# Performance work log

Hardware: AMD Instinct MI355X
Metric: run time of the kernel (lower is better)

Reference implementation:

```python
import jax, jax.numpy as jnp
import numpy as np

BETA = 0.25  # commitment_beta


def setup_inputs() -> dict:
    key = jax.random.key(0)
    k1, k2 = jax.random.split(key)
    x = jax.random.normal(k1, (16, 256, 32, 32), dtype=jnp.float32)
    # codebook weight: (n_embed + 1, embed_dim); last row is the padding idx (zeros)
    weight = jax.random.normal(k2, (8193, 256), dtype=jnp.float32) * 0.05
    weight = weight.at[-1].set(0.0)
    return {"x": x, "weight": weight}


def reference(x, weight):
    # Eval-mode forward of VectorQuantize2 (accept_image_fmap=True, no EMA update).
    B, C, H, W = x.shape
    xf = jnp.transpose(x, (0, 2, 3, 1)).reshape(B, H * W, C)  # b (h w) c
    emb = weight[:-1]  # [N, C], drop padding row
    # squared euclidean distance; argmin identical to torch.cdist argmin
    d2 = (
        jnp.sum(xf * xf, axis=-1, keepdims=True)
        - 2.0 * jnp.einsum("bnc,kc->bnk", xf, emb)
        + jnp.sum(emb * emb, axis=-1)
    )  # [B, HW, N]
    code = jnp.argmin(d2, axis=-1)  # [B, HW]
    x_q = emb[code]  # [B, HW, C]
    loss = BETA * jnp.mean((jax.lax.stop_gradient(x_q) - xf) ** 2) + jnp.mean(
        (x_q - jax.lax.stop_gradient(xf)) ** 2
    )
    # straight-through estimator
    xq_st = xf + jax.lax.stop_gradient(x_q - xf)
    xq_out = jnp.transpose(xq_st.reshape(B, H, W, C), (0, 3, 1, 2))  # b c h w
    code_out = code.reshape(B, H, W)
    return xq_out, loss, code_out
```

## Files before the change

### kernel.cpp

```cpp
#include <hip/hip_runtime.h>
#include <hip/hip_bf16.h>


#define N_ROWS   16384
#define KCODES   8192
#define DIM      256
#define LOSS_OFF 4194304
#define CODE_OFF 4194305
#define MARGIN_ACC 0.006f

typedef _Float16 half8  __attribute__((ext_vector_type(8)));
typedef _Float16 half4v __attribute__((ext_vector_type(4)));
typedef float    float4v __attribute__((ext_vector_type(4)));
typedef unsigned long long u64;

__device__ __forceinline__ unsigned umax32(unsigned a, unsigned b) { return a > b ? a : b; }
__device__ __forceinline__ unsigned umin32(unsigned a, unsigned b) { return a < b ? a : b; }
__device__ __forceinline__ void gll16(const _Float16* g, _Float16* l) {
  __builtin_amdgcn_global_load_lds((const __attribute__((address_space(1))) void*)g,
                                   (__attribute__((address_space(3))) void*)l, 16, 0, 0);
}


__global__ __launch_bounds__(256) void k_prep(const float* __restrict__ x, _Float16* __restrict__ xh,
                                              const float* __restrict__ wt, _Float16* __restrict__ eh,
                                              float* __restrict__ en2c) {
  __shared__ __align__(16) _Float16 ls[8192];
  __shared__ float es[32];
  int t = threadIdx.x;
  if (blockIdx.x < 256) {
    int blk = blockIdx.x;
    int row = t & 63;
    int s   = t >> 6;
    int r   = blk * 64 + row;
    int b   = r >> 10;
    int n   = r & 1023;
    const float* xb = x + (size_t)b * 262144 + n;
    int r7 = r & 7, rl = r & 127;
    size_t tb = (size_t)(r >> 7) * 32768;
    for (int j = 0; j < 8; ++j) {
      int g = s + 4 * j;
      int chunk = g >> 3, kg = g & 7;
      half8 h;
#pragma unroll
      for (int i = 0; i < 8; ++i) h[i] = (_Float16)xb[(size_t)(g * 8 + i) * 1024];
      int p = kg ^ r7;
      *(half8*)&xh[tb + (size_t)chunk * 8192 + rl * 64 + p * 8] = h;
    }
  } else {
    int blk  = blockIdx.x - 256;
    int lane = t & 63, wv = t >> 6;
    int k0 = blk * 32;
    const float* wb = wt + (size_t)k0 * 256;
    for (int i = 0; i < 8; ++i) {
      int lin = i * 1024 + t * 4;
      float4v v = *(const float4v*)&wb[lin];
      half4v h; float ss = 0.f;
#pragma unroll
      for (int j = 0; j < 4; ++j) { h[j] = (_Float16)v[j]; ss = fmaf(v[j], v[j], ss); }
      *(half4v*)&ls[lin] = h;
#pragma unroll
      for (int d = 32; d; d >>= 1) ss += __shfl_xor(ss, d);
      if (lane == 0) es[i * 4 + wv] = ss;
    }
    __syncthreads();
    size_t tb = (size_t)(k0 >> 7) * 32768;
    for (int i = 0; i < 4; ++i) {
      int u = i * 256 + t;
      int code_l = u >> 5;
      int cu = u & 31, chunk = cu >> 3, p = cu & 7;
      int kgl = k0 + code_l;
      int kg = p ^ (kgl & 7);
      half8 h = *(half8*)&ls[code_l * 256 + chunk * 64 + kg * 8];
      *(half8*)&eh[tb + (size_t)chunk * 8192 + (size_t)(kgl & 127) * 64 + p * 8] = h;
    }
    if (t < 32) en2c[k0 + t] = 32.0f - 0.5f * es[t];
  }
}

__global__ __launch_bounds__(256) void k_gemm(const _Float16* __restrict__ xh, const _Float16* __restrict__ eh,
                                              const float* __restrict__ en2c,
                                              u64* __restrict__ top2) {
  __shared__ __align__(16) _Float16 As[8192];
  __shared__ __align__(16) _Float16 Bs[8192];
  int t    = threadIdx.x;
  int bx   = blockIdx.x;
  int by   = blockIdx.y;
  int lane = t & 63, w = t >> 6;
  int wr = w & 1, wc = w >> 1;
  int ln15 = lane & 15, q = lane >> 4;
  int q4 = q * 4;

  const _Float16* Ag = eh + (size_t)bx * 32768;
  const _Float16* Bg = xh + (size_t)by * 32768;

  int kwave = bx * 128 + wr * 64;
  float4v cin[4];
#pragma unroll
  for (int mi = 0; mi < 4; ++mi) cin[mi] = *(const float4v*)&en2c[kwave + mi * 16 + q4];

  float4v acc[4][4];
#pragma unroll
  for (int mi = 0; mi < 4; ++mi)
#pragma unroll
    for (int ni = 0; ni < 4; ++ni) acc[mi][ni] = cin[mi];

  int so = (w * 64 + lane) * 8;
  int lo = w * 512;

  for (int ch = 0; ch < 4; ++ch) {
    if (ch) __syncthreads();
    const _Float16* ac = Ag + ch * 8192;
    const _Float16* bc = Bg + ch * 8192;
#pragma unroll
    for (int i = 0; i < 4; ++i) {
      gll16(ac + i * 2048 + so, As + i * 2048 + lo);
      gll16(bc + i * 2048 + so, Bs + i * 2048 + lo);
    }
    __syncthreads();
#pragma unroll
    for (int ks = 0; ks < 2; ++ks) {
      half8 af[4], bf[4];
#pragma unroll
      for (int mi = 0; mi < 4; ++mi) {
        int row = wr * 64 + mi * 16 + ln15;
        af[mi] = *(const half8*)&As[(row * 8 + ((ks * 4 + q) ^ (row & 7))) * 8];
      }
#pragma unroll
      for (int ni = 0; ni < 4; ++ni) {
        int row = wc * 64 + ni * 16 + ln15;
        bf[ni] = *(const half8*)&Bs[(row * 8 + ((ks * 4 + q) ^ (row & 7))) * 8];
      }
#pragma unroll
      for (int mi = 0; mi < 4; ++mi)
#pragma unroll
        for (int ni = 0; ni < 4; ++ni)
          acc[mi][ni] = __builtin_amdgcn_mfma_f32_16x16x32_f16(af[mi], bf[ni], acc[mi][ni], 0, 0, 0);
    }
  }

  __syncthreads();
  u64* ep = (u64*)(void*)As;
  int ibase = wr * 64 + q4;

#pragma unroll
  for (int ni = 0; ni < 4; ++ni) {
    unsigned hi[8], lo2[8];
#pragma unroll
    for (int j = 0; j < 8; ++j) {
      int mi = j >> 1, rb = (j & 1) * 2;
      unsigned p0 = (__float_as_uint(acc[mi][ni][rb])     & 0xFFFFFF80u) | (unsigned)(ibase + mi * 16 + rb);
      unsigned p1 = (__float_as_uint(acc[mi][ni][rb + 1]) & 0xFFFFFF80u) | (unsigned)(ibase + mi * 16 + rb + 1);
      hi[j] = umax32(p0, p1); lo2[j] = umin32(p0, p1);
    }
#pragma unroll
    for (int st = 4; st; st >>= 1)
#pragma unroll
      for (int j = 0; j < 8; ++j) if (j < st) {
        unsigned nb = umax32(hi[j], hi[j + st]);
        unsigned ns = umax32(umin32(hi[j], hi[j + st]), umax32(lo2[j], lo2[j + st]));
        hi[j] = nb; lo2[j] = ns;
      }
    unsigned b = hi[0], s = lo2[0];
#pragma unroll
    for (int d = 16; d < 64; d <<= 1) {
      unsigned ob = __shfl_xor(b, d);
      unsigned os = __shfl_xor(s, d);
      unsigned ns = umax32(umin32(b, ob), umax32(s, os));
      b = umax32(b, ob); s = ns;
    }
    if (q == 0) {
      int rl = wc * 64 + ni * 16 + ln15;
      ep[rl * 2 + wr] = ((u64)b << 32) | s;
    }
  }
  __syncthreads();
  if (t < 128) {
    u64 A = ep[t * 2 + 0], B = ep[t * 2 + 1];
    unsigned a0 = (unsigned)(A >> 32), a1 = (unsigned)A;
    unsigned b0 = (unsigned)(B >> 32), b1 = (unsigned)B;
    unsigned best = umax32(a0, b0);
    unsigned sec  = umax32(umin32(a0, b0), umax32(a1, b1));
    top2[((size_t)by * 128 + t) * 64 + bx] = ((u64)best << 32) | sec;
  }
}

__global__ __launch_bounds__(256) void k_refine_out(const u64* __restrict__ top2,
                                                    const float* __restrict__ x, const float* __restrict__ w,
                                                    float* __restrict__ out,
                                                    float* __restrict__ lacc, unsigned* __restrict__ cnt) {
  __shared__ float ec[32 * 261];
  __shared__ int   cds[32];
  __shared__ float part[4];
  int t    = threadIdx.x;
  int lane = t & 63, wv = t >> 6;
  int blk  = blockIdx.x;
  int row0 = blk * 32;
  int b = row0 >> 10, n0 = row0 & 1023;

  for (int j = 0; j < 8; ++j) {
    int rl  = wv + 4 * j;
    int row = row0 + rl;
    u64 e = top2[(size_t)row * 64 + lane];
    unsigned hi = (unsigned)(e >> 32), lo = (unsigned)e;
    unsigned mx = hi;
#pragma unroll
    for (int d = 1; d < 64; d <<= 1) mx = umax32(mx, __shfl_xor(mx, d));
    float fm = __uint_as_float(mx & 0xFFFFFF80u);
    float th = fm - MARGIN_ACC;
    bool c0 = __uint_as_float(hi & 0xFFFFFF80u) >= th;
    bool c1 = __uint_as_float(lo & 0xFFFFFF80u) >= th;
    u64 bal0 = __ballot(c0), bal1 = __ballot(c1);
    int kbest;
    if (__popcll(bal0) + __popcll(bal1) <= 1) {
      int l0 = __ffsll((unsigned long long)__ballot(hi == mx)) - 1;
      kbest = l0 * 128 + (int)(__shfl(hi, l0) & 127u);
    } else {
      int n = row & 1023;
      const float* xr = x + (size_t)b * 262144 + n;
      float4v ex;
#pragma unroll
      for (int i = 0; i < 4; ++i) ex[i] = xr[(size_t)(lane * 4 + i) * 1024];
      double bs = 1e300; int bk = 0x7fffffff;
      for (int pass = 0; pass < 2; ++pass) {
        u64 bal = pass ? bal1 : bal0;
        unsigned src = pass ? lo : hi;
        while (bal) {
          int l = __ffsll((unsigned long long)bal) - 1;
          bal &= bal - 1;
          int kc = l * 128 + (int)(__shfl(src, l) & 127u);
          float4v wv4 = *(const float4v*)&w[(size_t)kc * DIM + lane * 4];
          double s = 0.0;
#pragma unroll
          for (int i = 0; i < 4; ++i) { double ev = (double)wv4[i]; s += ev * (ev - 2.0 * (double)ex[i]); }
#pragma unroll
          for (int d = 1; d < 64; d <<= 1) s += __shfl_xor(s, d);
          if (s < bs || (s == bs && kc < bk)) { bs = s; bk = kc; }
        }
      }
      kbest = bk;
    }
    if (lane == 0) { cds[rl] = kbest; out[CODE_OFF + row] = (float)kbest; }
  }
  __syncthreads();

  {
    int rr = t >> 6;
    int c4 = (t & 63) * 4;
    for (int j = 0; j < 8; ++j) {
      int r = rr + 4 * j;
      float4v v = *(const float4v*)&w[(size_t)cds[r] * DIM + c4];
#pragma unroll
      for (int i = 0; i < 4; ++i) ec[r * 261 + c4 + i] = v[i];
    }
  }
  __syncthreads();
  float ls = 0.f;
  int r2 = t & 31;
  int cg = t >> 5;
  const size_t base = (size_t)b * 262144 + n0 + r2;
  for (int j = 0; j < 32; ++j) {
    int c = cg * 32 + j;
    float v  = ec[r2 * 261 + c];
    size_t a = base + (size_t)c * 1024;
    float xv = x[a];
    out[a] = v;
    float d = v - xv;
    ls = fmaf(d, d, ls);
  }
#pragma unroll
  for (int d = 32; d; d >>= 1) ls += __shfl_xor(ls, d);
  if (lane == 0) part[wv] = ls;
  __syncthreads();
  if (t == 0) {
    atomicAdd(lacc, part[0] + part[1] + part[2] + part[3]);
    __threadfence();
    unsigned old = atomicAdd(cnt, 1u);
    if (old == 511u) {
      __threadfence();
      out[LOSS_OFF] = 1.25f * (*(volatile float*)lacc) / 4194304.0f;
    }
  }
}

extern "C" void kernel_launch(void* const* d_in, const int* in_sizes, int n_in,
                              void* d_out, int out_size, void* d_ws, size_t ws_size,
                              hipStream_t stream) {
  const float* x = (const float*)d_in[0];
  const float* w = (const float*)d_in[1];
  float* out = (float*)d_out;
  char* ws = (char*)d_ws;
  _Float16* xh   = (_Float16*)(ws);
  _Float16* eh   = (_Float16*)(ws + 8388608);
  float*    en2c = (float*)(ws + 12582912);
  u64*      top2 = (u64*)(ws + 12615680);
  float*    lacc = (float*)(ws + 21004288);
  unsigned* cnt  = (unsigned*)(ws + 21004292);

  hipMemsetAsync(lacc, 0, 8, stream);
  k_prep<<<512, 256, 0, stream>>>(x, xh, w, eh, en2c);
  k_gemm<<<dim3(64, 128), 256, 0, stream>>>(xh, eh, en2c, top2);
  k_refine_out<<<512, 256, 0, stream>>>(top2, x, w, out, lacc, cnt);
}
```

Measured before the change: 190.1 us.

## Coalesce x transpose via LDS, split refine/output kernels, drop memset

The x-to-fp16 prep now reads x with coalesced float4 loads, transposes through padded shared memory and writes the swizzled tiles. The refine+output kernel is split in two: a highly parallel refine kernel (one wave per row, 4096 blocks) that writes codes to workspace, and an output kernel that gathers codebook rows into a swizzled LDS tile for 64 rows and writes the output plus loss. The loss accumulator reset moves from a memset into k_prep. This adds one kernel launch and an extra small code round trip through global memory.

```diff
diff --git a/kernel.cpp b/kernel.cpp
--- a/kernel.cpp
+++ b/kernel.cpp
@@ -24,28 +24,41 @@
 
 __global__ __launch_bounds__(256) void k_prep(const float* __restrict__ x, _Float16* __restrict__ xh,
                                               const float* __restrict__ wt, _Float16* __restrict__ eh,
-                                              float* __restrict__ en2c) {
+                                              float* __restrict__ en2c,
+                                              float* __restrict__ lacc, unsigned* __restrict__ cnt) {
   __shared__ __align__(16) _Float16 ls[8192];
   __shared__ float es[32];
   int t = threadIdx.x;
   if (blockIdx.x < 256) {
-    int blk = blockIdx.x;
-    int row = t & 63;
-    int s   = t >> 6;
-    int r   = blk * 64 + row;
-    int b   = r >> 10;
-    int n   = r & 1023;
-    const float* xb = x + (size_t)b * 262144 + n;
-    int r7 = r & 7, rl = r & 127;
-    size_t tb = (size_t)(r >> 7) * 32768;
-    for (int j = 0; j < 8; ++j) {
-      int g = s + 4 * j;
-      int chunk = g >> 3, kg = g & 7;
-      half8 h;
-#pragma unroll
-      for (int i = 0; i < 8; ++i) h[i] = (_Float16)xb[(size_t)(g * 8 + i) * 1024];
-      int p = kg ^ r7;
-      *(half8*)&xh[tb + (size_t)chunk * 8192 + rl * 64 + p * 8] = h;
+    if (blockIdx.x == 0 && t == 0) { *lacc = 0.f; *cnt = 0u; }
+    int blk  = blockIdx.x;
+    int row0 = blk * 64;
+    int b    = row0 >> 10;
+    int n0   = row0 & 1023;
+    const float* xb = x + (size_t)b * 262144 + n0;
+    _Float16 (*lsx)[72] = (_Float16(*)[72])ls;
+    int c_l = t >> 2;
+    int ng0 = t & 3;
+    for (int cc = 0; cc < 4; ++cc) {
+      if (cc) __syncthreads();
+#pragma unroll
+      for (int p = 0; p < 4; ++p) {
+        int ng = ng0 + 4 * p;
+        float4v v = *(const float4v*)&xb[(size_t)(cc * 64 + c_l) * 1024 + ng * 4];
+#pragma unroll
+        for (int k = 0; k < 4; ++k) lsx[ng * 4 + k][c_l] = (_Float16)v[k];
+      }
+      __syncthreads();
+#pragma unroll
+      for (int p2 = 0; p2 < 2; ++p2) {
+        int unit = t + 256 * p2;
+        int rl64 = unit >> 3, p7 = unit & 7;
+        int r = row0 + rl64;
+        int kg = p7 ^ (r & 7);
+        half8 h = *(const half8*)&lsx[rl64][kg * 8];
+        size_t tb = (size_t)(r >> 7) * 32768;
+        *(half8*)&xh[tb + (size_t)cc * 8192 + (size_t)(r & 127) * 64 + p7 * 8] = h;
+      }
     }
   } else {
     int blk  = blockIdx.x - 256;
@@ -185,83 +198,80 @@
   }
 }
 
-__global__ __launch_bounds__(256) void k_refine_out(const u64* __restrict__ top2,
-                                                    const float* __restrict__ x, const float* __restrict__ w,
-                                                    float* __restrict__ out,
-                                                    float* __restrict__ lacc, unsigned* __restrict__ cnt) {
-  __shared__ float ec[32 * 261];
-  __shared__ int   cds[32];
-  __shared__ float part[4];
+__global__ __launch_bounds__(256) void k_refine(const u64* __restrict__ top2,
+                                                const float* __restrict__ x, const float* __restrict__ w,
+                                                int* __restrict__ code, float* __restrict__ out) {
+  int t = threadIdx.x, lane = t & 63, wv = t >> 6;
+  int row = blockIdx.x * 4 + wv;
+  u64 e = top2[(size_t)row * 64 + lane];
+  unsigned hi = (unsigned)(e >> 32), lo = (unsigned)e;
+  unsigned mx = hi;
+#pragma unroll
+  for (int d = 1; d < 64; d <<= 1) mx = umax32(mx, __shfl_xor(mx, d));
+  float fm = __uint_as_float(mx & 0xFFFFFF80u);
+  float th = fm - MARGIN_ACC;
+  bool c0 = __uint_as_float(hi & 0xFFFFFF80u) >= th;
+  bool c1 = __uint_as_float(lo & 0xFFFFFF80u) >= th;
+  u64 bal0 = __ballot(c0), bal1 = __ballot(c1);
+  int kbest;
+  if (__popcll(bal0) + __popcll(bal1) <= 1) {
+    int l0 = __ffsll((unsigned long long)__ballot(hi == mx)) - 1;
+    kbest = l0 * 128 + (int)(__shfl(hi, l0) & 127u);
+  } else {
+    int b = row >> 10, n = row & 1023;
+    const float* xr = x + (size_t)b * 262144 + n;
+    float4v ex;
+#pragma unroll
+    for (int i = 0; i < 4; ++i) ex[i] = xr[(size_t)(lane * 4 + i) * 1024];
+    double bs = 1e300; int bk = 0x7fffffff;
+    for (int pass = 0; pass < 2; ++pass) {
+      u64 bal = pass ? bal1 : bal0;
+      unsigned src = pass ? lo : hi;
+      while (bal) {
+        int l = __ffsll((unsigned long long)bal) - 1;
+        bal &= bal - 1;
+        int kc = l * 128 + (int)(__shfl(src, l) & 127u);
+        float4v wv4 = *(const float4v*)&w[(size_t)kc * DIM + lane * 4];
+        double s = 0.0;
+#pragma unroll
+        for (int i = 0; i < 4; ++i) { double ev = (double)wv4[i]; s += ev * (ev - 2.0 * (double)ex[i]); }
+#pragma unroll
+        for (int d = 1; d < 64; d <<= 1) s += __shfl_xor(s, d);
+        if (s < bs || (s == bs && kc < bk)) { bs = s; bk = kc; }
+      }
+    }
+    kbest = bk;
+  }
+  if (lane == 0) { code[row] = kbest; out[CODE_OFF + row] = (float)kbest; }
+}
+
+__global__ __launch_bounds__(256) void k_out(const int* __restrict__ code, const float* __restrict__ w,
+                                             const float* __restrict__ x, float* __restrict__ out,
+                                             float* __restrict__ lacc, unsigned* __restrict__ cnt) {
+  __shared__ float ec[64 * 256];
   int t    = threadIdx.x;
   int lane = t & 63, wv = t >> 6;
   int blk  = blockIdx.x;
-  int row0 = blk * 32;
+  int row0 = blk * 64;
   int b = row0 >> 10, n0 = row0 & 1023;
 
-  for (int j = 0; j < 8; ++j) {
-    int rl  = wv + 4 * j;
-    int row = row0 + rl;
-    u64 e = top2[(size_t)row * 64 + lane];
-    unsigned hi = (unsigned)(e >> 32), lo = (unsigned)e;
-    unsigned mx = hi;
-#pragma unroll
-    for (int d = 1; d < 64; d <<= 1) mx = umax32(mx, __shfl_xor(mx, d));
-    float fm = __uint_as_float(mx & 0xFFFFFF80u);
-    float th = fm - MARGIN_ACC;
-    bool c0 = __uint_as_float(hi & 0xFFFFFF80u) >= th;
-    bool c1 = __uint_as_float(lo & 0xFFFFFF80u) >= th;
-    u64 bal0 = __ballot(c0), bal1 = __ballot(c1);
-    int kbest;
-    if (__popcll(bal0) + __popcll(bal1) <= 1) {
-      int l0 = __ffsll((unsigned long long)__ballot(hi == mx)) - 1;
-      kbest = l0 * 128 + (int)(__shfl(hi, l0) & 127u);
-    } else {
-      int n = row & 1023;
-      const float* xr = x + (size_t)b * 262144 + n;
-      float4v ex;
-#pragma unroll
-      for (int i = 0; i < 4; ++i) ex[i] = xr[(size_t)(lane * 4 + i) * 1024];
-      double bs = 1e300; int bk = 0x7fffffff;
-      for (int pass = 0; pass < 2; ++pass) {
-        u64 bal = pass ? bal1 : bal0;
-        unsigned src = pass ? lo : hi;
-        while (bal) {
-          int l = __ffsll((unsigned long long)bal) - 1;
-          bal &= bal - 1;
-          int kc = l * 128 + (int)(__shfl(src, l) & 127u);
-          float4v wv4 = *(const float4v*)&w[(size_t)kc * DIM + lane * 4];
-          double s = 0.0;
-#pragma unroll
-          for (int i = 0; i < 4; ++i) { double ev = (double)wv4[i]; s += ev * (ev - 2.0 * (double)ex[i]); }
-#pragma unroll
-          for (int d = 1; d < 64; d <<= 1) s += __shfl_xor(s, d);
-          if (s < bs || (s == bs && kc < bk)) { bs = s; bk = kc; }
-        }
-      }
-      kbest = bk;
-    }
-    if (lane == 0) { cds[rl] = kbest; out[CODE_OFF + row] = (float)kbest; }
-  }
-  __syncthreads();
-
-  {
-    int rr = t >> 6;
-    int c4 = (t & 63) * 4;
-    for (int j = 0; j < 8; ++j) {
-      int r = rr + 4 * j;
-      float4v v = *(const float4v*)&w[(size_t)cds[r] * DIM + c4];
-#pragma unroll
-      for (int i = 0; i < 4; ++i) ec[r * 261 + c4 + i] = v[i];
-    }
-  }
-  __syncthreads();
+  int kc = code[row0 + lane];
+  const float* wr = w + (size_t)kc * 256;
+  int sw = lane & 31;
+#pragma unroll 4
+  for (int i = 0; i < 16; ++i) {
+    int c4 = (wv * 16 + i) * 4;
+    float4v v = *(const float4v*)&wr[c4];
+#pragma unroll
+    for (int k = 0; k < 4; ++k) ec[lane * 256 + ((c4 + k) ^ sw)] = v[k];
+  }
+  __syncthreads();
+
   float ls = 0.f;
-  int r2 = t & 31;
-  int cg = t >> 5;
-  const size_t base = (size_t)b * 262144 + n0 + r2;
-  for (int j = 0; j < 32; ++j) {
-    int c = cg * 32 + j;
-    float v  = ec[r2 * 261 + c];
+  const size_t base = (size_t)b * 262144 + n0 + lane;
+  for (int j = 0; j < 64; ++j) {
+    int c = wv * 64 + j;
+    float v = ec[lane * 256 + (c ^ sw)];
     size_t a = base + (size_t)c * 1024;
     float xv = x[a];
     out[a] = v;
@@ -270,13 +280,14 @@
   }
 #pragma unroll
   for (int d = 32; d; d >>= 1) ls += __shfl_xor(ls, d);
-  if (lane == 0) part[wv] = ls;
+  __syncthreads();
+  if (lane == 0) ec[wv] = ls;
   __syncthreads();
   if (t == 0) {
-    atomicAdd(lacc, part[0] + part[1] + part[2] + part[3]);
+    atomicAdd(lacc, ec[0] + ec[1] + ec[2] + ec[3]);
     __threadfence();
     unsigned old = atomicAdd(cnt, 1u);
-    if (old == 511u) {
+    if (old == 255u) {
       __threadfence();
       out[LOSS_OFF] = 1.25f * (*(volatile float*)lacc) / 4194304.0f;
     }
@@ -294,11 +305,12 @@
   _Float16* eh   = (_Float16*)(ws + 8388608);
   float*    en2c = (float*)(ws + 12582912);
   u64*      top2 = (u64*)(ws + 12615680);
-  float*    lacc = (float*)(ws + 21004288);
-  unsigned* cnt  = (unsigned*)(ws + 21004292);
-
-  hipMemsetAsync(lacc, 0, 8, stream);
-  k_prep<<<512, 256, 0, stream>>>(x, xh, w, eh, en2c);
+  int*      codep = (int*)(ws + 21004288);
+  float*    lacc = (float*)(ws + 21069824);
+  unsigned* cnt  = (unsigned*)(ws + 21069828);
+
+  k_prep<<<512, 256, 0, stream>>>(x, xh, w, eh, en2c, lacc, cnt);
   k_gemm<<<dim3(64, 128), 256, 0, stream>>>(xh, eh, en2c, top2);
-  k_refine_out<<<512, 256, 0, stream>>>(top2, x, w, out, lacc, cnt);
-}
+  k_refine<<<4096, 256, 0, stream>>>(top2, x, w, codep, out);
+  k_out<<<256, 256, 0, stream>>>(codep, w, x, out, lacc, cnt);
+}
```

After: 180.3 us. 1.05x faster.
